# Kernel optimization log

Measured on AMD Instinct MI355X. Metric: run time of the kernel, lower is better.

Reference implementation:

```python
import jax, jax.numpy as jnp
import numpy as np

VOCAB = 50000          # max binary columnId
N_NUM = 5000           # numerical feature ids = 1..5000
N_CAT = VOCAB + 1 - N_NUM  # categorical table rows (incl. padding row 0)
D = 128
B, L = 512, 512


def setup_inputs() -> dict:
    key = jax.random.key(0)
    k1, k2, k3, k4, k5 = jax.random.split(key, 5)
    feature_ids = jax.random.randint(k1, (B, L), 0, VOCAB + 1)
    feature_values = jax.random.normal(k2, (B, L), dtype=jnp.float32)
    cat_table = jax.random.normal(k3, (N_CAT, D), dtype=jnp.float32) * 0.02
    cat_table = cat_table.at[0].set(0.0)  # padding_idx=0
    num_weight = jax.random.normal(k4, (N_NUM, D), dtype=jnp.float32) * 0.02
    num_bias = jax.random.normal(k5, (N_NUM, D), dtype=jnp.float32) * 0.02
    # lookup buffers, exactly as built in __init__ with numerical ids = 1..N_NUM
    input_to_numeric = np.zeros(VOCAB + 1, dtype=np.int64)
    num_ids = np.arange(1, N_NUM + 1)
    input_to_numeric[num_ids] = np.arange(1, N_NUM + 1)
    input_to_categorical = np.zeros(VOCAB + 1, dtype=np.int64)
    cat_ids = np.where(input_to_numeric == 0)[0]
    input_to_categorical[cat_ids[1:]] = np.arange(1, cat_ids.size)
    return {
        "feature_ids": feature_ids,
        "feature_values": feature_values,
        "cat_table": cat_table,
        "num_weight": num_weight,
        "num_bias": num_bias,
        "input_to_numeric": jnp.asarray(input_to_numeric),
        "input_to_categorical": jnp.asarray(input_to_categorical),
    }


def reference(feature_ids, feature_values, cat_table, num_weight, num_bias,
              input_to_numeric, input_to_categorical):
    # numerical mask: isin(feature_ids, numerical_feature_ids) == nonzero mapped idx
    n_idx = input_to_numeric[feature_ids]                 # [B,L], 1..N_NUM or 0
    numerical_mask = n_idx > 0                            # [B,L]
    # numerical path: weight[id] * value + bias[id]  (1-based mapped -> 0-based row)
    n_row = jnp.maximum(n_idx - 1, 0)                     # [B,L]
    num_emb = num_weight[n_row] * feature_values[..., None] + num_bias[n_row]  # [B,L,D]
    # categorical path: route numerical positions to padding id 0
    cat_features = jnp.where(numerical_mask, 0, feature_ids)
    c_idx = input_to_categorical[cat_features]            # [B,L]
    cat_emb = cat_table[c_idx]                            # [B,L,D]
    # merge
    return jnp.where(numerical_mask[..., None], num_emb, cat_emb)
```

## Files before the change

### kernel.cpp

```cpp
#include <hip/hip_runtime.h>


constexpr int D  = 128;
constexpr int BL = 512 * 512;

__global__ __launch_bounds__(256) void emb_kernel(
    const int*    __restrict__ feature_ids,
    const float*  __restrict__ feature_values,
    const float*  __restrict__ cat_table,
    const float*  __restrict__ num_weight,
    const float*  __restrict__ num_bias,
    const int*    __restrict__ input_to_numeric,
    const int*    __restrict__ input_to_categorical,
    float*        __restrict__ out)
{
    const int t   = blockIdx.x * 256 + threadIdx.x;
    const int pos = t >> 5;
    const int sub = t & 31;

    const int id    = feature_ids[pos];
    const int n_idx = input_to_numeric[id];

    float4 r;
    if (n_idx > 0) {
        const float v = feature_values[pos];
        const long long off = (long long)(n_idx - 1) * D + sub * 4;
        const float4 w = *(const float4*)(num_weight + off);
        const float4 b = *(const float4*)(num_bias   + off);
        r.x = fmaf(w.x, v, b.x);
        r.y = fmaf(w.y, v, b.y);
        r.z = fmaf(w.z, v, b.z);
        r.w = fmaf(w.w, v, b.w);
    } else {
        const int c = input_to_categorical[id];
        r = *(const float4*)(cat_table + (long long)c * D + sub * 4);
    }

    *(float4*)(out + (long long)pos * D + sub * 4) = r;
}

extern "C" void kernel_launch(void* const* d_in, const int* in_sizes, int n_in,
                              void* d_out, int out_size, void* d_ws, size_t ws_size,
                              hipStream_t stream) {
    const int*   feature_ids          = (const int*)  d_in[0];
    const float* feature_values       = (const float*)d_in[1];
    const float* cat_table            = (const float*)d_in[2];
    const float* num_weight           = (const float*)d_in[3];
    const float* num_bias             = (const float*)d_in[4];
    const int*   input_to_numeric     = (const int*)  d_in[5];
    const int*   input_to_categorical = (const int*)  d_in[6];
    float*       out                  = (float*)      d_out;

    const int blocks = (BL * 32) / 256;
    emb_kernel<<<blocks, 256, 0, stream>>>(
        feature_ids, feature_values, cat_table, num_weight, num_bias,
        input_to_numeric, input_to_categorical, out);
}
```

Measured before the change: 197.6 us.

## Resolve routes once per block in shared memory and use nontemporal stores

Each block now covers 32 positions instead of 8. The first 32 threads resolve the id lookups (numeric vs categorical route, plus the value) once into shared memory. Each thread then issues four independent gathers before writing, using nontemporal stores for the 128 MB output. This removes the redundant per-thread index loads and increases memory-level parallelism, at the cost of a block-wide barrier and a serialized lookup phase.

```diff
diff --git a/kernel.cpp b/kernel.cpp
--- a/kernel.cpp
+++ b/kernel.cpp
@@ -1,8 +1,16 @@
 #include <hip/hip_runtime.h>
 
 
-constexpr int D  = 128;
-constexpr int BL = 512 * 512;
+constexpr int D   = 128;
+constexpr int BL  = 512 * 512;
+constexpr int POS_PER_BLOCK = 32;
+
+typedef float vfloat4 __attribute__((ext_vector_type(4)));
+
+union F4 {
+    float4  h;
+    vfloat4 n;
+};
 
 __global__ __launch_bounds__(256) void emb_kernel(
     const int*    __restrict__ feature_ids,
@@ -14,29 +22,49 @@
     const int*    __restrict__ input_to_categorical,
     float*        __restrict__ out)
 {
-    const int t   = blockIdx.x * 256 + threadIdx.x;
-    const int pos = t >> 5;
-    const int sub = t & 31;
+    __shared__ int   s_route[POS_PER_BLOCK];
+    __shared__ float s_val[POS_PER_BLOCK];
 
-    const int id    = feature_ids[pos];
-    const int n_idx = input_to_numeric[id];
+    const int tid  = threadIdx.x;
+    const int base = blockIdx.x * POS_PER_BLOCK;
 
-    float4 r;
-    if (n_idx > 0) {
-        const float v = feature_values[pos];
-        const long long off = (long long)(n_idx - 1) * D + sub * 4;
-        const float4 w = *(const float4*)(num_weight + off);
-        const float4 b = *(const float4*)(num_bias   + off);
-        r.x = fmaf(w.x, v, b.x);
-        r.y = fmaf(w.y, v, b.y);
-        r.z = fmaf(w.z, v, b.z);
-        r.w = fmaf(w.w, v, b.w);
-    } else {
-        const int c = input_to_categorical[id];
-        r = *(const float4*)(cat_table + (long long)c * D + sub * 4);
+    if (tid < POS_PER_BLOCK) {
+        const int id = feature_ids[base + tid];
+        s_val[tid]   = feature_values[base + tid];
+        const int n  = input_to_numeric[id];
+        s_route[tid] = (n > 0) ? -n : input_to_categorical[id];
+    }
+    __syncthreads();
+
+    F4 r[4];
+#pragma unroll
+    for (int pass = 0; pass < 4; ++pass) {
+        const int idx = pass * 256 + tid;
+        const int p   = idx >> 5;
+        const int sub = idx & 31;
+        const int route = s_route[p];
+        if (route < 0) {
+            const long long off = (long long)(-route - 1) * D + sub * 4;
+            const float4 w = *(const float4*)(num_weight + off);
+            const float4 b = *(const float4*)(num_bias   + off);
+            const float  v = s_val[p];
+            r[pass].h.x = fmaf(w.x, v, b.x);
+            r[pass].h.y = fmaf(w.y, v, b.y);
+            r[pass].h.z = fmaf(w.z, v, b.z);
+            r[pass].h.w = fmaf(w.w, v, b.w);
+        } else {
+            r[pass].h = *(const float4*)(cat_table + (long long)route * D + sub * 4);
+        }
     }
 
-    *(float4*)(out + (long long)pos * D + sub * 4) = r;
+#pragma unroll
+    for (int pass = 0; pass < 4; ++pass) {
+        const int idx = pass * 256 + tid;
+        const int p   = idx >> 5;
+        const int sub = idx & 31;
+        vfloat4* dst = (vfloat4*)(out + (long long)(base + p) * D + sub * 4);
+        __builtin_nontemporal_store(r[pass].n, dst);
+    }
 }
 
 extern "C" void kernel_launch(void* const* d_in, const int* in_sizes, int n_in,
@@ -51,7 +79,7 @@
     const int*   input_to_categorical = (const int*)  d_in[6];
     float*       out                  = (float*)      d_out;
 
-    const int blocks = (BL * 32) / 256;
+    const int blocks = BL / POS_PER_BLOCK;
     emb_kernel<<<blocks, 256, 0, stream>>>(
         feature_ids, feature_values, cat_table, num_weight, num_bias,
         input_to_numeric, input_to_categorical, out);
```

Result: faster. 186.2 us (-5.8%).
